# Kernel tuning notes

Hardware: AMD Instinct MI355X
Metric: run time of the kernel (lower is better)

## Reference

```python
import jax, jax.numpy as jnp
import numpy as np

B, L, D, H = 2, 4096, 512, 8
HD = D // H  # head_dim = 64


def setup_inputs() -> dict:
    key = jax.random.key(0)
    ks = jax.random.split(key, 5)
    s = 0.02
    return {
        "x": jax.random.normal(ks[0], (B, L, D), dtype=jnp.float32),
        "w_qkv": jax.random.normal(ks[1], (D, 3 * D), dtype=jnp.float32) * s,
        "b_qkv": jax.random.normal(ks[2], (3 * D,), dtype=jnp.float32) * s,
        "w_o": jax.random.normal(ks[3], (D, D), dtype=jnp.float32) * s,
        "b_o": jax.random.normal(ks[4], (D,), dtype=jnp.float32) * s,
    }


def reference(x, w_qkv, b_qkv, w_o, b_o):
    b, l, _ = x.shape
    # QKV projection, then split heads: [B, L, 3D] -> [B, H, L, 3*HD]
    qkv = x @ w_qkv + b_qkv
    qkv = qkv.reshape(b, l, H, 3 * HD).transpose(0, 2, 1, 3)
    q, k, v = jnp.split(qkv, 3, axis=-1)  # each [B, H, L, HD]
    scale = 1.0 / jnp.sqrt(jnp.asarray(HD, dtype=q.dtype))
    # full score matrix [B, H, L, L], softmax in float32 (matches .float() cast)
    scores = jnp.einsum('bhld,bhsd->bhls', q, k) * scale
    attn = jax.nn.softmax(scores.astype(jnp.float32), axis=-1).astype(q.dtype)
    values = jnp.einsum('bhls,bhsd->bhld', attn, v)  # [B, H, L, HD]
    values = values.transpose(0, 2, 1, 3).reshape(b, l, D)
    return values @ w_o + b_o
```

## Files before the change

### kernel.cpp

```cpp
#include <hip/hip_runtime.h>


#define B_  2
#define L_  4096
#define D_  512
#define H_  8
#define HD_ 64
#define BH_ (B_*H_)
#define M_  (B_*L_)
#define QKVN (3*D_)
#define HEADSZ (BH_*L_*HD_)

typedef unsigned short ushort;
typedef unsigned int uint;
typedef __bf16 bf16x8 __attribute__((ext_vector_type(8)));
typedef float  f32x4  __attribute__((ext_vector_type(4)));
typedef float  f32x16 __attribute__((ext_vector_type(16)));

typedef const __attribute__((address_space(1))) void g_void;
typedef __attribute__((address_space(3))) void l_void;

#define C2_ 0.18033688011112042f

#if __has_builtin(__builtin_amdgcn_exp2f)
#define FEXP2(x) __builtin_amdgcn_exp2f(x)
#else
#define FEXP2(x) exp2f(x)
#endif

__device__ __forceinline__ ushort f2bf(float f) {
    __bf16 h = (__bf16)f;
    return __builtin_bit_cast(ushort, h);
}

__device__ __forceinline__ uint pack2(float lo, float hi) {
    return (uint)f2bf(lo) | ((uint)f2bf(hi) << 16);
}

__global__ __launch_bounds__(256)
void prep_k(const float* __restrict__ x, ushort* __restrict__ xb,
            const float* __restrict__ wq, ushort* __restrict__ wtq,
            const float* __restrict__ wo, ushort* __restrict__ wto)
{
    int bid = blockIdx.x, tid = threadIdx.x;
    if (bid < 4096) {
        int idx = bid * 256 + tid;
        float4 v = ((const float4*)x)[idx];
        ushort4 o; o.x = f2bf(v.x); o.y = f2bf(v.y); o.z = f2bf(v.z); o.w = f2bf(v.w);
        ((ushort4*)xb)[idx] = o;
    } else if (bid < 7168) {
        int idx = (bid - 4096) * 256 + tid;
        int c = idx / D_, r = idx % D_;
        wtq[idx] = f2bf(wq[r * QKVN + c]);
    } else {
        int idx = (bid - 7168) * 256 + tid;
        int c = idx / D_, r = idx % D_;
        wto[idx] = f2bf(wo[r * D_ + c]);
    }
}

#define TP 66
__global__ __launch_bounds__(256)
void transpose_v(const ushort* __restrict__ V, ushort* __restrict__ VT) {
    __shared__ ushort T[64 * TP];
    const int tid = threadIdx.x;
    const int bh = blockIdx.y;
    const int l0 = blockIdx.x * 64;
    const int base = bh * (L_ * HD_);
    #pragma unroll
    for (int i = 0; i < 2; i++) {
        int c = i * 256 + tid;
        int l = c >> 3, dc = (c & 7) * 8;
        uint4 v = *(const uint4*)&V[base + (l0 + l) * HD_ + dc];
        uint* p = (uint*)&T[l * TP + dc];
        p[0] = v.x; p[1] = v.y; p[2] = v.z; p[3] = v.w;
    }
    __syncthreads();
    #pragma unroll
    for (int p = 0; p < 2; p++) {
        int c = p * 256 + tid;
        int d = c >> 3, lb = c & 7;
        ushort tmp[8];
        #pragma unroll
        for (int j = 0; j < 8; j++) tmp[j] = T[(lb * 8 + j) * TP + d];
        *(uint4*)&VT[base + d * L_ + l0 + lb * 8] = *(uint4*)tmp;
    }
}

__global__ __launch_bounds__(256)
void gemm_bt(const ushort* __restrict__ A, const ushort* __restrict__ Bt,
             const float* __restrict__ bias, void* __restrict__ out,
             int M, int N, int K, int mode)
{
    __shared__ ushort As[128 * 32];
    __shared__ ushort Bs[128 * 32];

    const int tid  = threadIdx.x;
    const int lane = tid & 63;
    const int wid  = tid >> 6;
    const int wm   = wid >> 1, wn = wid & 1;
    const int lr   = lane & 15;
    const int quad = lane >> 4;
    const int tm = blockIdx.x, tn = blockIdx.y;

    f32x4 acc[4][4] = {};
    const int arow = tm * 128;
    const int brow = tn * 128;

    for (int k0 = 0; k0 < K; k0 += 32) {
        #pragma unroll
        for (int i = 0; i < 2; i++) {
            int c   = i * 256 + tid;
            int row = c >> 2;
            int kk  = (c & 3) * 8;
            __builtin_amdgcn_global_load_lds(
                (g_void*)&A[(size_t)(arow + row) * K + k0 + kk],
                (l_void*)&As[c * 8], 16, 0, 0);
            __builtin_amdgcn_global_load_lds(
                (g_void*)&Bt[(size_t)(brow + row) * K + k0 + kk],
                (l_void*)&Bs[c * 8], 16, 0, 0);
        }
        __syncthreads();

        bf16x8 af[4], bfr[4];
        #pragma unroll
        for (int t = 0; t < 4; t++) {
            af [t] = *(const bf16x8*)&As[(wm * 64 + t * 16 + lr) * 32 + quad * 8];
            bfr[t] = *(const bf16x8*)&Bs[(wn * 64 + t * 16 + lr) * 32 + quad * 8];
        }
        #pragma unroll
        for (int mt = 0; mt < 4; mt++)
            #pragma unroll
            for (int nt = 0; nt < 4; nt++)
                acc[mt][nt] = __builtin_amdgcn_mfma_f32_16x16x32_bf16(
                    af[mt], bfr[nt], acc[mt][nt], 0, 0, 0);
        __syncthreads();
    }

    #pragma unroll
    for (int nt = 0; nt < 4; nt++) {
        int col = tn * 128 + wn * 64 + nt * 16 + lr;
        float bv = bias[col];
        #pragma unroll
        for (int mt = 0; mt < 4; mt++) {
            #pragma unroll
            for (int r = 0; r < 4; r++) {
                int row = tm * 128 + wm * 64 + mt * 16 + quad * 4 + r;
                float v = acc[mt][nt][r] + bv;
                if (mode == 0) {
                    ((float*)out)[(size_t)row * N + col] = v;
                } else {
                    int d = col & 63;
                    int g = col >> 6;
                    int which = g % 3;
                    int h = g / 3;
                    int b = row >> 12;
                    int l = row & (L_ - 1);
                    if (which == 0) v *= C2_;
                    ((ushort*)out)[which * HEADSZ + (((b * H_ + h) * L_ + l) * HD_) + d]
                        = f2bf(v);
                }
            }
        }
    }
}

__global__ __launch_bounds__(256)
void attn_k(const ushort* __restrict__ Q, const ushort* __restrict__ K,
            const ushort* __restrict__ VT, ushort* __restrict__ O)
{
    __shared__ __align__(16) ushort Ksm[2][64 * 64];
    __shared__ __align__(16) ushort Vsm[4][64 * 64];
    __shared__ float Linv[4][32];

    const int tid  = threadIdx.x;
    const int lane = tid & 63;
    const int wid  = tid >> 6;
    const int l31  = lane & 31;
    const int hi   = lane >> 5;

    const int wg  = blockIdx.x;
    const int xcd = wg & 7, sl = wg >> 3;
    const int bh  = (xcd << 1) | (sl >> 5);
    const int q0  = (sl & 31) * 128;
    const size_t base = (size_t)bh * (L_ * HD_);

    const int sr0 = tid >> 3,        sr1 = (tid + 256) >> 3;
    const int sc0 = ((tid & 7) ^ (sr0 & 7)) * 8;
    const int sc1 = ((tid & 7) ^ (sr1 & 7)) * 8;
    const ushort* Kg0 = K  + base + sr0 * HD_ + sc0;
    const ushort* Kg1 = K  + base + sr1 * HD_ + sc1;
    const ushort* Vg0 = VT + base + (size_t)sr0 * L_ + sc0;
    const ushort* Vg1 = VT + base + (size_t)sr1 * L_ + sc1;

    bf16x8 qf[4];
    {
        const ushort* qp = Q + base + (size_t)(q0 + wid * 32 + l31) * HD_ + hi * 8;
        #pragma unroll
        for (int ks = 0; ks < 4; ks++) qf[ks] = *(const bf16x8*)(qp + ks * 16);
    }

    const int swz = (l31 & 7) << 4;
    int cbe[4];
    #pragma unroll
    for (int ks = 0; ks < 4; ks++) cbe[ks] = ((ks * 32 + hi * 16) ^ swz) >> 1;
    const int kr0 = l31 * 64, kr1 = (32 + l31) * 64;

    f32x16 o0 = {}, o1 = {};
    f32x16 sEA, sEB, sOA, sOB;
    float l4[4] = {0.f, 0.f, 0.f, 0.f};

    auto STAGE = [&](int tt) {
        const size_t ko = (size_t)tt * 64 * HD_;
        const int    vo = tt * 64;
        ushort* kb = &Ksm[tt & 1][0];
        ushort* vb = &Vsm[tt & 3][0];
        __builtin_amdgcn_global_load_lds((g_void*)(Kg0 + ko), (l_void*)(kb + tid * 8),        16, 0, 0);
        __builtin_amdgcn_global_load_lds((g_void*)(Kg1 + ko), (l_void*)(kb + tid * 8 + 2048), 16, 0, 0);
        __builtin_amdgcn_global_load_lds((g_void*)(Vg0 + vo), (l_void*)(vb + tid * 8),        16, 0, 0);
        __builtin_amdgcn_global_load_lds((g_void*)(Vg1 + vo), (l_void*)(vb + tid * 8 + 2048), 16, 0, 0);
    };

    auto QK = [&](int tt, f32x16& SA, f32x16& SB) {
        const ushort* kb = &Ksm[tt & 1][0];
        SA = f32x16{}; SB = f32x16{};
        #pragma unroll
        for (int ks = 0; ks < 4; ks++) {
            bf16x8 k0 = *(const bf16x8*)&kb[kr0 + cbe[ks]];
            bf16x8 k1 = *(const bf16x8*)&kb[kr1 + cbe[ks]];
            SA = __builtin_amdgcn_mfma_f32_32x32x16_bf16(k0, qf[ks], SA, 0, 0, 0);
            SB = __builtin_amdgcn_mfma_f32_32x32x16_bf16(k1, qf[ks], SB, 0, 0, 0);
        }
    };

    auto SMPV = [&](int tp, f32x16& SA, f32x16& SB) {
        const ushort* vb = &Vsm[tp & 3][0];
        #pragma unroll
        for (int i = 0; i < 16; i++) { SA[i] = FEXP2(SA[i]); SB[i] = FEXP2(SB[i]); }
        #pragma unroll
        for (int i = 0; i < 16; i++) l4[i & 3] += SA[i] + SB[i];
        #pragma unroll
        for (int ks = 0; ks < 4; ks++) {
            const f32x16& P = (ks >> 1) ? SB : SA;
            const int r0 = 8 * (ks & 1);
            uint a0 = pack2(P[r0 + 0], P[r0 + 1]);
            uint a1 = pack2(P[r0 + 2], P[r0 + 3]);
            uint b0 = pack2(P[r0 + 4], P[r0 + 5]);
            uint b1 = pack2(P[r0 + 6], P[r0 + 7]);
            asm("v_permlane32_swap_b32 %0, %1" : "+v"(a0), "+v"(b0));
            asm("v_permlane32_swap_b32 %0, %1" : "+v"(a1), "+v"(b1));
            uint4 w; w.x = a0; w.y = a1; w.z = b0; w.w = b1;
            bf16x8 pa = __builtin_bit_cast(bf16x8, w);
            bf16x8 v0 = *(const bf16x8*)&vb[kr0 + cbe[ks]];
            bf16x8 v1 = *(const bf16x8*)&vb[kr1 + cbe[ks]];
            o0 = __builtin_amdgcn_mfma_f32_32x32x16_bf16(pa, v0, o0, 0, 0, 0);
            o1 = __builtin_amdgcn_mfma_f32_32x32x16_bf16(pa, v1, o1, 0, 0, 0);
        }
    };

    STAGE(0);

    for (int t = 0; t < L_ / 64; t += 2) {
        __syncthreads();
        STAGE(t + 1);
        QK(t, sEA, sEB);
        if (t > 0) SMPV(t - 1, sOA, sOB);
        __syncthreads();
        if (t + 2 < L_ / 64) STAGE(t + 2);
        QK(t + 1, sOA, sOB);
        SMPV(t, sEA, sEB);
    }
    SMPV(L_ / 64 - 1, sOA, sOB);

    float lp = (l4[0] + l4[1]) + (l4[2] + l4[3]);
    lp += __shfl_xor(lp, 32, 64);
    if (hi == 0) Linv[wid][l31] = 1.0f / lp;

    const int b = bh >> 3, h = bh & 7;
    #pragma unroll
    for (int r = 0; r < 16; r++) {
        const int qrl = (r & 3) + 8 * (r >> 2) + 4 * hi;
        const float inv = Linv[wid][qrl];
        const size_t row = (size_t)(b * L_ + q0 + wid * 32 + qrl) * D_ + h * HD_ + l31;
        O[row]      = f2bf(o0[r] * inv);
        O[row + 32] = f2bf(o1[r] * inv);
    }
}

extern "C" void kernel_launch(void* const* d_in, const int* in_sizes, int n_in,
                              void* d_out, int out_size, void* d_ws, size_t ws_size,
                              hipStream_t stream)
{
    const float* x     = (const float*)d_in[0];
    const float* w_qkv = (const float*)d_in[1];
    const float* b_qkv = (const float*)d_in[2];
    const float* w_o   = (const float*)d_in[3];
    const float* b_o   = (const float*)d_in[4];

    char* ws = (char*)d_ws;
    size_t o = 0;
    ushort* xb   = (ushort*)(ws + o); o += (size_t)M_ * D_ * 2;
    ushort* qkv  = (ushort*)(ws + o); o += (size_t)3 * HEADSZ * 2;
    ushort* attn = (ushort*)(ws + o); o += (size_t)M_ * D_ * 2;
    ushort* wtq  = (ushort*)(ws + o); o += (size_t)QKVN * D_ * 2;
    ushort* wto  = (ushort*)(ws + o);
    ushort* vt   = xb;

    hipLaunchKernelGGL(prep_k, dim3(8192), dim3(256), 0, stream,
                       x, xb, w_qkv, wtq, w_o, wto);
    hipLaunchKernelGGL(gemm_bt, dim3(M_ / 128, QKVN / 128), dim3(256), 0, stream,
                       xb, wtq, b_qkv, (void*)qkv, M_, QKVN, D_, 1);
    hipLaunchKernelGGL(transpose_v, dim3(L_ / 64, BH_), dim3(256), 0, stream,
                       qkv + 2 * HEADSZ, vt);
    hipLaunchKernelGGL(attn_k, dim3(512), dim3(256), 0, stream,
                       qkv, qkv + HEADSZ, vt, attn);
    hipLaunchKernelGGL(gemm_bt, dim3(M_ / 128, D_ / 128), dim3(256), 0, stream,
                       attn, wto, b_o, d_out, M_, D_, D_, 0);
}
```

Measured before the change: 212.5 us.

## Load K tiles directly into registers instead of staging through LDS

```diff
diff --git a/kernel.cpp b/kernel.cpp
--- a/kernel.cpp
+++ b/kernel.cpp
@@ -169,7 +169,6 @@
 void attn_k(const ushort* __restrict__ Q, const ushort* __restrict__ K,
             const ushort* __restrict__ VT, ushort* __restrict__ O)
 {
-    __shared__ __align__(16) ushort Ksm[2][64 * 64];
     __shared__ __align__(16) ushort Vsm[4][64 * 64];
     __shared__ float Linv[4][32];
 
@@ -188,8 +187,6 @@
     const int sr0 = tid >> 3,        sr1 = (tid + 256) >> 3;
     const int sc0 = ((tid & 7) ^ (sr0 & 7)) * 8;
     const int sc1 = ((tid & 7) ^ (sr1 & 7)) * 8;
-    const ushort* Kg0 = K  + base + sr0 * HD_ + sc0;
-    const ushort* Kg1 = K  + base + sr1 * HD_ + sc1;
     const ushort* Vg0 = VT + base + (size_t)sr0 * L_ + sc0;
     const ushort* Vg1 = VT + base + (size_t)sr1 * L_ + sc1;
 
@@ -200,6 +197,8 @@
         for (int ks = 0; ks < 4; ks++) qf[ks] = *(const bf16x8*)(qp + ks * 16);
     }
 
+    const ushort* Kp = K + base + (size_t)l31 * HD_ + hi * 8;
+
     const int swz = (l31 & 7) << 4;
     int cbe[4];
     #pragma unroll
@@ -208,28 +207,31 @@
 
     f32x16 o0 = {}, o1 = {};
     f32x16 sEA, sEB, sOA, sOB;
+    bf16x8 kE[8], kO[8];
     float l4[4] = {0.f, 0.f, 0.f, 0.f};
 
-    auto STAGE = [&](int tt) {
-        const size_t ko = (size_t)tt * 64 * HD_;
-        const int    vo = tt * 64;
-        ushort* kb = &Ksm[tt & 1][0];
+    auto STAGE_V = [&](int tt) {
+        const int vo = tt * 64;
         ushort* vb = &Vsm[tt & 3][0];
-        __builtin_amdgcn_global_load_lds((g_void*)(Kg0 + ko), (l_void*)(kb + tid * 8),        16, 0, 0);
-        __builtin_amdgcn_global_load_lds((g_void*)(Kg1 + ko), (l_void*)(kb + tid * 8 + 2048), 16, 0, 0);
         __builtin_amdgcn_global_load_lds((g_void*)(Vg0 + vo), (l_void*)(vb + tid * 8),        16, 0, 0);
         __builtin_amdgcn_global_load_lds((g_void*)(Vg1 + vo), (l_void*)(vb + tid * 8 + 2048), 16, 0, 0);
     };
 
-    auto QK = [&](int tt, f32x16& SA, f32x16& SB) {
-        const ushort* kb = &Ksm[tt & 1][0];
+    auto LOADK = [&](int tt, bf16x8* kr) {
+        const ushort* kp = Kp + (size_t)tt * 64 * HD_;
+        #pragma unroll
+        for (int ks = 0; ks < 4; ks++) {
+            kr[ks]     = *(const bf16x8*)(kp + ks * 16);
+            kr[ks + 4] = *(const bf16x8*)(kp + 32 * HD_ + ks * 16);
+        }
+    };
+
+    auto QK = [&](const bf16x8* kr, f32x16& SA, f32x16& SB) {
         SA = f32x16{}; SB = f32x16{};
         #pragma unroll
         for (int ks = 0; ks < 4; ks++) {
-            bf16x8 k0 = *(const bf16x8*)&kb[kr0 + cbe[ks]];
-            bf16x8 k1 = *(const bf16x8*)&kb[kr1 + cbe[ks]];
-            SA = __builtin_amdgcn_mfma_f32_32x32x16_bf16(k0, qf[ks], SA, 0, 0, 0);
-            SB = __builtin_amdgcn_mfma_f32_32x32x16_bf16(k1, qf[ks], SB, 0, 0, 0);
+            SA = __builtin_amdgcn_mfma_f32_32x32x16_bf16(kr[ks],     qf[ks], SA, 0, 0, 0);
+            SB = __builtin_amdgcn_mfma_f32_32x32x16_bf16(kr[ks + 4], qf[ks], SB, 0, 0, 0);
         }
     };
 
@@ -258,16 +260,20 @@
         }
     };
 
-    STAGE(0);
+    STAGE_V(0);
+    LOADK(0, kE);
+    LOADK(1, kO);
 
     for (int t = 0; t < L_ / 64; t += 2) {
         __syncthreads();
-        STAGE(t + 1);
-        QK(t, sEA, sEB);
+        STAGE_V(t + 1);
+        QK(kE, sEA, sEB);
+        if (t + 2 < L_ / 64) LOADK(t + 2, kE);
         if (t > 0) SMPV(t - 1, sOA, sOB);
         __syncthreads();
-        if (t + 2 < L_ / 64) STAGE(t + 2);
-        QK(t + 1, sOA, sOB);
+        if (t + 2 < L_ / 64) STAGE_V(t + 2);
+        QK(kO, sOA, sOB);
+        if (t + 3 < L_ / 64) LOADK(t + 3, kO);
         SMPV(t, sEA, sEB);
     }
     SMPV(L_ / 64 - 1, sOA, sOB);
```

New measurement: 334.8 us. 1.58x slower.
